# Optimization experiments

Measured on AMD Instinct MI355X. Metric: run time of the kernel, lower is better.

Reference implementation:

```python
import jax, jax.numpy as jnp
import numpy as np

N = 100000   # nodes
E = 1600000  # edges (no self loops; module adds them)
D = 128      # in_dim == out_dim
BN_EPS = 1e-5
NORM_EPS = 1e-12


def setup_inputs() -> dict:
    key = jax.random.key(0)
    ks = jax.random.split(key, 9)
    x = jax.random.normal(ks[0], (N, D), jnp.float32)
    src = jax.random.randint(ks[1], (E,), 0, N, dtype=jnp.int32)
    dst = jax.random.randint(ks[2], (E,), 0, N, dtype=jnp.int32)
    dst = jnp.where(dst == src, (dst + 1) % N, dst)  # no pre-existing self loops
    edge_index = jnp.stack([src, dst], axis=0)
    edge_w = jax.random.uniform(ks[3], (E, 2), jnp.float32)
    # MySAGEConv.linear: Linear(2*D -> D) since concat=True
    W_lin = jax.random.normal(ks[4], (2 * D, D), jnp.float32) * (1.0 / np.sqrt(2 * D))
    b_lin = jnp.zeros((D,), jnp.float32)
    # BatchNorm1d(D)
    gamma = jnp.ones((D,), jnp.float32)
    beta = jnp.zeros((D,), jnp.float32)
    # PositionEmbedding(2, D): Linear(2->D//2, no bias), ReLU, Linear(D//2->D, no bias)
    pos_w1 = jax.random.normal(ks[5], (2, D // 2), jnp.float32) * 0.1
    pos_w2 = jax.random.normal(ks[6], (D // 2, D), jnp.float32) * 0.1
    return {"x": x, "edge_index": edge_index, "edge_w": edge_w,
            "W_lin": W_lin, "b_lin": b_lin, "gamma": gamma, "beta": beta,
            "pos_w1": pos_w1, "pos_w2": pos_w2}


def reference(x, edge_index, edge_w, W_lin, b_lin, gamma, beta, pos_w1, pos_w2):
    src, dst = edge_index[0], edge_index[1]
    # Position embedding is computed by the block but DISCARDED inside MySAGEConv.forward,
    # because add_remaining_self_loops(edge_index, None, 1, N) overwrites edge_weight with None.
    _pe = jnp.maximum(edge_w @ pos_w1, 0.0) @ pos_w2  # [E, D], unused (faithful to bug)
    # add_remaining_self_loops: append a self loop for every node
    loops = jnp.arange(N, dtype=src.dtype)
    src_f = jnp.concatenate([src, loops])
    dst_f = jnp.concatenate([dst, loops])
    # message = x_j (edge_weight is None); aggr = 'mean' scatter over destinations
    msg = x[src_f]                                           # [E+N, D] gather
    summed = jax.ops.segment_sum(msg, dst_f, num_segments=N)  # [N, D] scatter-add
    cnt = jax.ops.segment_sum(jnp.ones((E + N, 1), x.dtype), dst_f, num_segments=N)
    aggr = summed / cnt                                      # every node has >=1 (self loop)
    # update: concat + linear + L2 normalize
    h = jnp.concatenate([x, aggr], axis=-1) @ W_lin + b_lin   # [N, D]
    h = h / jnp.maximum(jnp.linalg.norm(h, axis=-1, keepdims=True), NORM_EPS)
    # BatchNorm1d (training-mode batch stats, biased variance)
    mu = jnp.mean(h, axis=0)
    var = jnp.var(h, axis=0)
    h = (h - mu) * jax.lax.rsqrt(var + BN_EPS) * gamma + beta
    # residual (in_dim == out_dim) + ReLU
    return jnp.maximum(h + x, 0.0)
```

## Files before the change

### kernel.cpp

```cpp
#include <hip/hip_runtime.h>
#include <hip/hip_bf16.h>

typedef __attribute__((ext_vector_type(4))) float f32x4;
typedef __attribute__((ext_vector_type(8))) short short8;
typedef unsigned short u16;
typedef unsigned long long u64;

static __device__ __forceinline__ u16 f2bf(float f) {
    __hip_bfloat16 h = __float2bfloat16(f);
    return __builtin_bit_cast(u16, h);
}
static __device__ __forceinline__ float bf2f(u16 u) {
    unsigned int w = ((unsigned int)u) << 16;
    return __builtin_bit_cast(float, w);
}

__global__ void k_cvt(const float* __restrict__ x, u16* __restrict__ xb, int total8) {
    const float4* x4 = (const float4*)x;
    int stride = gridDim.x * blockDim.x;
    for (int i = blockIdx.x * blockDim.x + threadIdx.x; i < total8; i += stride) {
        float4 a = x4[i * 2], b = x4[i * 2 + 1];
        union { u16 u[8]; short8 v; } o;
        o.u[0] = f2bf(a.x); o.u[1] = f2bf(a.y); o.u[2] = f2bf(a.z); o.u[3] = f2bf(a.w);
        o.u[4] = f2bf(b.x); o.u[5] = f2bf(b.y); o.u[6] = f2bf(b.z); o.u[7] = f2bf(b.w);
        *(short8*)(xb + (size_t)i * 8) = o.v;
    }
}

__global__ void k_deg(const int* __restrict__ dst, int* __restrict__ deg,
                      int E, int chunk) {
    const int NX = 8;
    int group = blockIdx.x & (NX - 1);
    int bseq = blockIdx.x >> 3;
    int nblk = gridDim.x >> 3;
    int lo = group * chunk, hi = lo + chunk;
    int E4 = E >> 2;
    const int4* d4 = (const int4*)dst;
    int stride = nblk * blockDim.x;
    int gid = bseq * blockDim.x + threadIdx.x;
    for (int i = gid; i < E4; i += stride) {
        int4 v = d4[i];
        if (v.x >= lo && v.x < hi) atomicAdd(&deg[v.x], 1);
        if (v.y >= lo && v.y < hi) atomicAdd(&deg[v.y], 1);
        if (v.z >= lo && v.z < hi) atomicAdd(&deg[v.z], 1);
        if (v.w >= lo && v.w < hi) atomicAdd(&deg[v.w], 1);
    }
    if (group == 0) {
        for (int e = E4 * 4 + gid; e < E; e += stride)
            atomicAdd(&deg[dst[e]], 1);
    }
}

__global__ void k_scan_a(const int* __restrict__ deg, int* __restrict__ bsum, int n) {
    __shared__ int s[256];
    int tid = threadIdx.x;
    int i = blockIdx.x * 256 + tid;
    s[tid] = (i < n) ? deg[i] : 0;
    __syncthreads();
    for (int ofs = 128; ofs > 0; ofs >>= 1) {
        if (tid < ofs) s[tid] += s[tid + ofs];
        __syncthreads();
    }
    if (tid == 0) bsum[blockIdx.x] = s[0];
}

__global__ void k_scan_b(const int* __restrict__ bsum, int* __restrict__ boff, int nb,
                         int* __restrict__ offN) {
    __shared__ int s[512];
    int tid = threadIdx.x;
    int v = (tid < nb) ? bsum[tid] : 0;
    s[tid] = v;
    __syncthreads();
    for (int ofs = 1; ofs < 512; ofs <<= 1) {
        int t = (tid >= ofs) ? s[tid - ofs] : 0;
        __syncthreads();
        s[tid] += t;
        __syncthreads();
    }
    if (tid < nb) boff[tid] = s[tid] - v;
    if (tid == nb - 1) offN[0] = s[tid];
}

__global__ void k_scan_c(const int* __restrict__ deg, const int* __restrict__ boff,
                         int* __restrict__ off, int* __restrict__ cur, int n) {
    __shared__ int s[256];
    int tid = threadIdx.x;
    int i = blockIdx.x * 256 + tid;
    int v = (i < n) ? deg[i] : 0;
    s[tid] = v;
    __syncthreads();
    for (int ofs = 1; ofs < 256; ofs <<= 1) {
        int t = (tid >= ofs) ? s[tid - ofs] : 0;
        __syncthreads();
        s[tid] += t;
        __syncthreads();
    }
    int excl = s[tid] - v + boff[blockIdx.x];
    if (i < n) { off[i] = excl; cur[i] = excl; }
}

__global__ void k_fill(const int* __restrict__ src, const int* __restrict__ dst,
                       int* __restrict__ cur, int* __restrict__ csr, int E, int chunk) {
    const int NX = 8;
    int group = blockIdx.x & (NX - 1);
    int bseq = blockIdx.x >> 3;
    int nblk = gridDim.x >> 3;
    int lo = group * chunk, hi = lo + chunk;
    int E4 = E >> 2;
    const int4* d4 = (const int4*)dst;
    int stride = nblk * blockDim.x;
    int gid = bseq * blockDim.x + threadIdx.x;
    for (int i = gid; i < E4; i += stride) {
        int4 v = d4[i];
        int e = i * 4;
        if (v.x >= lo && v.x < hi) { int p = atomicAdd(&cur[v.x], 1); csr[p] = src[e]; }
        if (v.y >= lo && v.y < hi) { int p = atomicAdd(&cur[v.y], 1); csr[p] = src[e + 1]; }
        if (v.z >= lo && v.z < hi) { int p = atomicAdd(&cur[v.z], 1); csr[p] = src[e + 2]; }
        if (v.w >= lo && v.w < hi) { int p = atomicAdd(&cur[v.w], 1); csr[p] = src[e + 3]; }
    }
    if (group == 0) {
        for (int e = E4 * 4 + gid; e < E; e += stride) {
            int d = dst[e];
            int p = atomicAdd(&cur[d], 1);
            csr[p] = src[e];
        }
    }
}

__global__ void k_aggr(const u16* __restrict__ xb, const int* __restrict__ off,
                       const int* __restrict__ csr, u16* __restrict__ aggr, int n) {
    int node = (blockIdx.x * blockDim.x + threadIdx.x) >> 6;
    if (node >= n) return;
    int lane = threadIdx.x & 63;
    int c = lane & 15;
    int j = lane >> 4;
    const short8* x8 = (const short8*)xb;
    int s0 = off[node], s1 = off[node + 1];
    float acc[8] = {0.f, 0.f, 0.f, 0.f, 0.f, 0.f, 0.f, 0.f};
    int e = s0;
    for (; e + 8 <= s1; e += 8) {
        short8 va = x8[(size_t)csr[e + j] * 16 + c];
        short8 vb = x8[(size_t)csr[e + j + 4] * 16 + c];
#pragma unroll
        for (int i = 0; i < 8; ++i)
            acc[i] += bf2f((u16)va[i]) + bf2f((u16)vb[i]);
    }
    {
        int r1 = e + j, r2 = e + j + 4;
        if (r1 < s1) {
            short8 va = x8[(size_t)csr[r1] * 16 + c];
#pragma unroll
            for (int i = 0; i < 8; ++i) acc[i] += bf2f((u16)va[i]);
        }
        if (r2 < s1) {
            short8 vb = x8[(size_t)csr[r2] * 16 + c];
#pragma unroll
            for (int i = 0; i < 8; ++i) acc[i] += bf2f((u16)vb[i]);
        }
    }
#pragma unroll
    for (int i = 0; i < 8; ++i) {
        acc[i] += __shfl_xor(acc[i], 16, 64);
        acc[i] += __shfl_xor(acc[i], 32, 64);
    }
    if (j == 0) {
        short8 sv = x8[(size_t)node * 16 + c];
        float inv = 1.0f / (float)(s1 - s0 + 1);
        short8 o;
#pragma unroll
        for (int i = 0; i < 8; ++i)
            o[i] = (short)f2bf((acc[i] + bf2f((u16)sv[i])) * inv);
        *(short8*)(aggr + (size_t)node * 128 + c * 8) = o;
    }
}

__global__ __launch_bounds__(512, 2) void k_linear(
    const u16* __restrict__ xb, u16* __restrict__ aggr ,
    const float* __restrict__ W, const float* __restrict__ b_lin,
    float* __restrict__ bnsum, float* __restrict__ bnsq,
    int n, int ntiles) {
    __shared__ u16 WT[32768];
    int tid = threadIdx.x;

    {
        int col = tid & 127;
        int kq0 = tid >> 7;
        int mask = (col & 15) << 3;
        char* base = (char*)WT + col * 512;
#pragma unroll
        for (int i = 0; i < 16; ++i) {
            int kq = kq0 + i * 4;
            int k = kq * 4;
            float w0 = W[(size_t)(k + 0) * 128 + col];
            float w1 = W[(size_t)(k + 1) * 128 + col];
            float w2 = W[(size_t)(k + 2) * 128 + col];
            float w3 = W[(size_t)(k + 3) * 128 + col];
            u64 q = (u64)f2bf(w0) | ((u64)f2bf(w1) << 16) |
                    ((u64)f2bf(w2) << 32) | ((u64)f2bf(w3) << 48);
            *(u64*)(base + ((8 * kq) ^ mask)) = q;
        }
    }
    __syncthreads();

    int wave = tid >> 6, l = tid & 63, lr = l & 15, lg = l >> 4;
    int pair = wave >> 1, hf = wave & 1;

    short8 breg[4][8];
#pragma unroll
    for (int ct2 = 0; ct2 < 4; ++ct2) {
        int col = hf * 64 + ct2 * 16 + lr;
        const char* rowp = (const char*)WT + col * 512;
        int mask = (col & 15) << 3;
#pragma unroll
        for (int kk = 0; kk < 8; ++kk) {
            int kb = kk * 64 + 8 * lg;
            u64 lo = *(const u64*)(rowp + (kb ^ mask));
            u64 hi = *(const u64*)(rowp + ((kb + 32) ^ mask));
            union { u64 q[2]; short8 v; } bu;
            bu.q[0] = lo; bu.q[1] = hi;
            breg[ct2][kk] = bu.v;
        }
    }
    __syncthreads();
    float* ssx = (float*)WT;

    float s1a[4] = {0, 0, 0, 0};
    float s2a[4] = {0, 0, 0, 0};
    int stride4 = gridDim.x * 4;

    for (int base = blockIdx.x * 4; base < ntiles; base += stride4) {
        int tile = base + pair;
        bool active = tile < ntiles;
        int rowA = tile * 16 + lr;
        bool rv = active && rowA < n;

        ushort4 xa[4], xc[4], ua[4], ub[4];
#pragma unroll
        for (int kk = 0; kk < 4; ++kk) {
            const u16* xp = xb + (size_t)rowA * 128 + kk * 32 + 4 * lg;
            xa[kk] = rv ? *(const ushort4*)xp : make_ushort4(0, 0, 0, 0);
            xc[kk] = rv ? *(const ushort4*)(xp + 16) : make_ushort4(0, 0, 0, 0);
        }
#pragma unroll
        for (int kk = 0; kk < 4; ++kk) {
            const u16* ap = aggr + (size_t)rowA * 128 + kk * 32 + 4 * lg;
            ua[kk] = rv ? *(const ushort4*)ap : make_ushort4(0, 0, 0, 0);
            ub[kk] = rv ? *(const ushort4*)(ap + 16) : make_ushort4(0, 0, 0, 0);
        }

        short8 av[8];
#pragma unroll
        for (int kk = 0; kk < 4; ++kk) {
            av[kk][0] = (short)xa[kk].x; av[kk][1] = (short)xa[kk].y;
            av[kk][2] = (short)xa[kk].z; av[kk][3] = (short)xa[kk].w;
            av[kk][4] = (short)xc[kk].x; av[kk][5] = (short)xc[kk].y;
            av[kk][6] = (short)xc[kk].z; av[kk][7] = (short)xc[kk].w;
            av[kk + 4][0] = (short)ua[kk].x; av[kk + 4][1] = (short)ua[kk].y;
            av[kk + 4][2] = (short)ua[kk].z; av[kk + 4][3] = (short)ua[kk].w;
            av[kk + 4][4] = (short)ub[kk].x; av[kk + 4][5] = (short)ub[kk].y;
            av[kk + 4][6] = (short)ub[kk].z; av[kk + 4][7] = (short)ub[kk].w;
        }

        f32x4 acc[4];
#pragma unroll
        for (int ct2 = 0; ct2 < 4; ++ct2) acc[ct2] = (f32x4){0.f, 0.f, 0.f, 0.f};
#pragma unroll
        for (int kk = 0; kk < 8; ++kk)
#pragma unroll
            for (int ct2 = 0; ct2 < 4; ++ct2)
                acc[ct2] = __builtin_amdgcn_mfma_f32_16x16x32_bf16(av[kk], breg[ct2][kk],
                                                                   acc[ct2], 0, 0, 0);

        float ss[4] = {0.f, 0.f, 0.f, 0.f};
#pragma unroll
        for (int ct2 = 0; ct2 < 4; ++ct2) {
            float bl = b_lin[hf * 64 + ct2 * 16 + lr];
#pragma unroll
            for (int q = 0; q < 4; ++q) {
                acc[ct2][q] += bl;
                ss[q] += acc[ct2][q] * acc[ct2][q];
            }
        }
#pragma unroll
        for (int m = 1; m < 16; m <<= 1) {
#pragma unroll
            for (int q = 0; q < 4; ++q) ss[q] += __shfl_xor(ss[q], m, 64);
        }
        if (lr == 0)
            *(float4*)&ssx[(pair * 2 + hf) * 16 + lg * 4] =
                make_float4(ss[0], ss[1], ss[2], ss[3]);
        __syncthreads();
        float4 oth = *(const float4*)&ssx[(pair * 2 + (1 - hf)) * 16 + lg * 4];
        float sc[4];
        sc[0] = 1.0f / fmaxf(sqrtf(ss[0] + oth.x), 1e-12f);
        sc[1] = 1.0f / fmaxf(sqrtf(ss[1] + oth.y), 1e-12f);
        sc[2] = 1.0f / fmaxf(sqrtf(ss[2] + oth.z), 1e-12f);
        sc[3] = 1.0f / fmaxf(sqrtf(ss[3] + oth.w), 1e-12f);
        __syncthreads();

        if (active) {
            int rq0 = tile * 16 + 4 * lg;
#pragma unroll
            for (int ct2 = 0; ct2 < 4; ++ct2) {
                float hn[4];
                float p1 = 0.f, p2 = 0.f;
#pragma unroll
                for (int q = 0; q < 4; ++q) {
                    hn[q] = acc[ct2][q] * sc[q];
                    if (rq0 + q >= n) hn[q] = 0.f;
                    p1 += hn[q]; p2 += hn[q] * hn[q];
                }
                s1a[ct2] += p1; s2a[ct2] += p2;
                ushort4 o;
                o.x = f2bf(hn[0]); o.y = f2bf(hn[1]); o.z = f2bf(hn[2]); o.w = f2bf(hn[3]);
                *(ushort4*)(aggr + (size_t)tile * 2048 + (hf * 4 + ct2) * 256 + l * 4) = o;
            }
        }
    }

#pragma unroll
    for (int ct2 = 0; ct2 < 4; ++ct2) {
        float v1 = s1a[ct2], v2 = s2a[ct2];
        v1 += __shfl_xor(v1, 16, 64); v1 += __shfl_xor(v1, 32, 64);
        v2 += __shfl_xor(v2, 16, 64); v2 += __shfl_xor(v2, 32, 64);
        if (lg == 0) {
            atomicAdd(&bnsum[hf * 64 + ct2 * 16 + lr], v1);
            atomicAdd(&bnsq[hf * 64 + ct2 * 16 + lr], v2);
        }
    }
}

__global__ __launch_bounds__(512) void k_final(
    const u16* __restrict__ hfrag, const float* __restrict__ x,
    const float* __restrict__ bnsum, const float* __restrict__ bnsq,
    const float* __restrict__ gamma, const float* __restrict__ beta,
    float* __restrict__ out, float invN, int n) {
    __shared__ float cf[256];
    __shared__ float ot[16 * 132];
    int tid = threadIdx.x;
    int tile = blockIdx.x;
    if (tid < 128) {
        float mu = bnsum[tid] * invN;
        float var = bnsq[tid] * invN - mu * mu;
        float a = gamma[tid] * rsqrtf(var + 1e-5f);
        cf[tid] = a;
        cf[128 + tid] = beta[tid] - mu * a;
    }
    __syncthreads();

    {
        int ct = tid >> 6, l = tid & 63;
        ushort4 hv = *(const ushort4*)(hfrag + (size_t)tile * 2048 + ct * 256 + l * 4);
        int col = ct * 16 + (l & 15);
        float a = cf[col], b = cf[128 + col];
        int rl0 = 4 * (l >> 4);
        ot[(rl0 + 0) * 132 + col] = bf2f(hv.x) * a + b;
        ot[(rl0 + 1) * 132 + col] = bf2f(hv.y) * a + b;
        ot[(rl0 + 2) * 132 + col] = bf2f(hv.z) * a + b;
        ot[(rl0 + 3) * 132 + col] = bf2f(hv.w) * a + b;
    }
    __syncthreads();

    {
        int rl = tid >> 5, c4 = tid & 31;
        int row = tile * 16 + rl;
        if (row < n) {
            float4 xv = *(const float4*)(x + (size_t)row * 128 + c4 * 4);
            const float* op = &ot[rl * 132 + c4 * 4];
            float4 o;
            o.x = fmaxf(op[0] + xv.x, 0.f);
            o.y = fmaxf(op[1] + xv.y, 0.f);
            o.z = fmaxf(op[2] + xv.z, 0.f);
            o.w = fmaxf(op[3] + xv.w, 0.f);
            *(float4*)(out + (size_t)row * 128 + c4 * 4) = o;
        }
    }
}

extern "C" void kernel_launch(void* const* d_in, const int* in_sizes, int n_in,
                              void* d_out, int out_size, void* d_ws, size_t ws_size,
                              hipStream_t stream) {
    const float* x     = (const float*)d_in[0];
    const int*   ei    = (const int*)d_in[1];
    const float* W     = (const float*)d_in[3];
    const float* b_lin = (const float*)d_in[4];
    const float* gamma = (const float*)d_in[5];
    const float* beta  = (const float*)d_in[6];
    int N = in_sizes[0] / 128;
    int E = in_sizes[1] / 2;
    const int* src = ei;
    const int* dst = ei + E;

    char* p = (char*)d_ws;
    auto alloc = [&](size_t bytes) { char* r = p; p += (bytes + 255) & ~(size_t)255; return r; };
    int*   deg   = (int*)alloc((size_t)N * 4);
    float* bnsum = (float*)alloc(128 * 4);
    float* bnsq  = (float*)alloc(128 * 4);
    size_t zspan = (char*)(bnsq + 128) - (char*)deg;
    int*   off   = (int*)alloc((size_t)(N + 1) * 4);
    int*   cur   = (int*)alloc((size_t)N * 4);
    int*   csr   = (int*)alloc((size_t)E * 4);
    int*   bsum  = (int*)alloc(512 * 4);
    int*   boff  = (int*)alloc(512 * 4);
    u16*   aggr  = (u16*)alloc((size_t)N * 128 * 2);

    u16* xbf = (u16*)d_out;

    hipMemsetAsync(deg, 0, zspan, stream);

    const int NGROUP = 8;
    int chunk = (N + NGROUP - 1) / NGROUP;

    k_cvt<<<2048, 256, 0, stream>>>(x, xbf, N * 16);
    k_deg<<<1024, 256, 0, stream>>>(dst, deg, E, chunk);
    int nb = (N + 255) / 256;
    k_scan_a<<<nb, 256, 0, stream>>>(deg, bsum, N);
    k_scan_b<<<1, 512, 0, stream>>>(bsum, boff, nb, off + N);
    k_scan_c<<<nb, 256, 0, stream>>>(deg, boff, off, cur, N);
    k_fill<<<1024, 256, 0, stream>>>(src, dst, cur, csr, E, chunk);
    k_aggr<<<(int)(((size_t)N * 64 + 255) / 256), 256, 0, stream>>>(xbf, off, csr, aggr, N);
    int ntiles = (N + 15) / 16;
    k_linear<<<256, 512, 0, stream>>>(xbf, aggr, W, b_lin, bnsum, bnsq, N, ntiles);
    k_final<<<ntiles, 512, 0, stream>>>(aggr, x, bnsum, bnsq, gamma, beta,
                                        (float*)d_out, 1.0f / (float)N, N);
}
```

Measured before the change: 306.0 us.

## Fuse convert and degree kernels, unroll gather by 16, double linear grid

Merges the bf16 conversion and degree-count kernels into one launch, splitting the grid by block index so both independent jobs run concurrently. The aggregation loop now gathers four neighbor rows per lane per iteration instead of two, giving more loads in flight, and uses a simple strided tail loop. The linear kernel grid is doubled from 256 to 512 blocks. Costs: the fused kernel divides the GPU between two different workloads, and the wider unroll raises register use.

```diff
diff --git a/kernel.cpp b/kernel.cpp
--- a/kernel.cpp
+++ b/kernel.cpp
@@ -3,6 +3,7 @@
 
 typedef __attribute__((ext_vector_type(4))) float f32x4;
 typedef __attribute__((ext_vector_type(8))) short short8;
+typedef __attribute__((ext_vector_type(4))) int i32x4;
 typedef unsigned short u16;
 typedef unsigned long long u64;
 
@@ -15,39 +16,40 @@
     return __builtin_bit_cast(float, w);
 }
 
-__global__ void k_cvt(const float* __restrict__ x, u16* __restrict__ xb, int total8) {
-    const float4* x4 = (const float4*)x;
-    int stride = gridDim.x * blockDim.x;
-    for (int i = blockIdx.x * blockDim.x + threadIdx.x; i < total8; i += stride) {
-        float4 a = x4[i * 2], b = x4[i * 2 + 1];
-        union { u16 u[8]; short8 v; } o;
-        o.u[0] = f2bf(a.x); o.u[1] = f2bf(a.y); o.u[2] = f2bf(a.z); o.u[3] = f2bf(a.w);
-        o.u[4] = f2bf(b.x); o.u[5] = f2bf(b.y); o.u[6] = f2bf(b.z); o.u[7] = f2bf(b.w);
-        *(short8*)(xb + (size_t)i * 8) = o.v;
-    }
-}
-
-__global__ void k_deg(const int* __restrict__ dst, int* __restrict__ deg,
-                      int E, int chunk) {
-    const int NX = 8;
-    int group = blockIdx.x & (NX - 1);
-    int bseq = blockIdx.x >> 3;
-    int nblk = gridDim.x >> 3;
-    int lo = group * chunk, hi = lo + chunk;
-    int E4 = E >> 2;
-    const int4* d4 = (const int4*)dst;
-    int stride = nblk * blockDim.x;
-    int gid = bseq * blockDim.x + threadIdx.x;
-    for (int i = gid; i < E4; i += stride) {
-        int4 v = d4[i];
-        if (v.x >= lo && v.x < hi) atomicAdd(&deg[v.x], 1);
-        if (v.y >= lo && v.y < hi) atomicAdd(&deg[v.y], 1);
-        if (v.z >= lo && v.z < hi) atomicAdd(&deg[v.z], 1);
-        if (v.w >= lo && v.w < hi) atomicAdd(&deg[v.w], 1);
-    }
-    if (group == 0) {
-        for (int e = E4 * 4 + gid; e < E; e += stride)
-            atomicAdd(&deg[dst[e]], 1);
+__global__ void k_pre(const float* __restrict__ x, u16* __restrict__ xb, int total8,
+                      const int* __restrict__ dst, int* __restrict__ deg,
+                      int E, int chunk, int cvtBlocks) {
+    int tid = threadIdx.x;
+    if ((int)blockIdx.x < cvtBlocks) {
+        const float4* x4 = (const float4*)x;
+        int stride = cvtBlocks * 256;
+        for (int i = blockIdx.x * 256 + tid; i < total8; i += stride) {
+            float4 a = x4[i * 2], b = x4[i * 2 + 1];
+            union { u16 u[8]; short8 v; } o;
+            o.u[0] = f2bf(a.x); o.u[1] = f2bf(a.y); o.u[2] = f2bf(a.z); o.u[3] = f2bf(a.w);
+            o.u[4] = f2bf(b.x); o.u[5] = f2bf(b.y); o.u[6] = f2bf(b.z); o.u[7] = f2bf(b.w);
+            *(short8*)(xb + (size_t)i * 8) = o.v;
+        }
+    } else {
+        int group = blockIdx.x & 7;
+        int bseq = (blockIdx.x - cvtBlocks) >> 3;
+        int nblk = (gridDim.x - cvtBlocks) >> 3;
+        int lo = group * chunk, hi = lo + chunk;
+        int E4 = E >> 2;
+        const int4* d4 = (const int4*)dst;
+        int stride = nblk * 256;
+        int gid = bseq * 256 + tid;
+        for (int i = gid; i < E4; i += stride) {
+            int4 v = d4[i];
+            if (v.x >= lo && v.x < hi) atomicAdd(&deg[v.x], 1);
+            if (v.y >= lo && v.y < hi) atomicAdd(&deg[v.y], 1);
+            if (v.z >= lo && v.z < hi) atomicAdd(&deg[v.z], 1);
+            if (v.w >= lo && v.w < hi) atomicAdd(&deg[v.w], 1);
+        }
+        if (group == 0) {
+            for (int e = E4 * 4 + gid; e < E; e += stride)
+                atomicAdd(&deg[dst[e]], 1);
+        }
     }
 }
 
@@ -138,25 +140,21 @@
     int s0 = off[node], s1 = off[node + 1];
     float acc[8] = {0.f, 0.f, 0.f, 0.f, 0.f, 0.f, 0.f, 0.f};
     int e = s0;
-    for (; e + 8 <= s1; e += 8) {
-        short8 va = x8[(size_t)csr[e + j] * 16 + c];
-        short8 vb = x8[(size_t)csr[e + j + 4] * 16 + c];
+    for (; e + 16 <= s1; e += 16) {
+        int r0 = csr[e + j], r1 = csr[e + j + 4], r2 = csr[e + j + 8], r3 = csr[e + j + 12];
+        short8 v0 = x8[(size_t)r0 * 16 + c];
+        short8 v1 = x8[(size_t)r1 * 16 + c];
+        short8 v2 = x8[(size_t)r2 * 16 + c];
+        short8 v3 = x8[(size_t)r3 * 16 + c];
 #pragma unroll
         for (int i = 0; i < 8; ++i)
-            acc[i] += bf2f((u16)va[i]) + bf2f((u16)vb[i]);
-    }
-    {
-        int r1 = e + j, r2 = e + j + 4;
-        if (r1 < s1) {
-            short8 va = x8[(size_t)csr[r1] * 16 + c];
-#pragma unroll
-            for (int i = 0; i < 8; ++i) acc[i] += bf2f((u16)va[i]);
-        }
-        if (r2 < s1) {
-            short8 vb = x8[(size_t)csr[r2] * 16 + c];
-#pragma unroll
-            for (int i = 0; i < 8; ++i) acc[i] += bf2f((u16)vb[i]);
-        }
+            acc[i] += (bf2f((u16)v0[i]) + bf2f((u16)v1[i])) +
+                      (bf2f((u16)v2[i]) + bf2f((u16)v3[i]));
+    }
+    for (int r = e + j; r < s1; r += 4) {
+        short8 v = x8[(size_t)csr[r] * 16 + c];
+#pragma unroll
+        for (int i = 0; i < 8; ++i) acc[i] += bf2f((u16)v[i]);
     }
 #pragma unroll
     for (int i = 0; i < 8; ++i) {
@@ -410,9 +408,9 @@
 
     const int NGROUP = 8;
     int chunk = (N + NGROUP - 1) / NGROUP;
-
-    k_cvt<<<2048, 256, 0, stream>>>(x, xbf, N * 16);
-    k_deg<<<1024, 256, 0, stream>>>(dst, deg, E, chunk);
+    const int CVTB = 768;
+
+    k_pre<<<CVTB + 1024, 256, 0, stream>>>(x, xbf, N * 16, dst, deg, E, chunk, CVTB);
     int nb = (N + 255) / 256;
     k_scan_a<<<nb, 256, 0, stream>>>(deg, bsum, N);
     k_scan_b<<<1, 512, 0, stream>>>(bsum, boff, nb, off + N);
@@ -420,7 +418,7 @@
     k_fill<<<1024, 256, 0, stream>>>(src, dst, cur, csr, E, chunk);
     k_aggr<<<(int)(((size_t)N * 64 + 255) / 256), 256, 0, stream>>>(xbf, off, csr, aggr, N);
     int ntiles = (N + 15) / 16;
-    k_linear<<<256, 512, 0, stream>>>(xbf, aggr, W, b_lin, bnsum, bnsq, N, ntiles);
+    k_linear<<<512, 512, 0, stream>>>(xbf, aggr, W, b_lin, bnsum, bnsq, N, ntiles);
     k_final<<<ntiles, 512, 0, stream>>>(aggr, x, bnsum, bnsq, gamma, beta,
                                         (float*)d_out, 1.0f / (float)N, N);
 }
```

New measurement: 310.2 us. Within noise of the previous version (+1.4%).
